# Performance work log

Hardware: AMD Instinct MI355X
Metric: run time of the kernel (lower is better)

Reference implementation:

```python
import jax, jax.numpy as jnp
import numpy as np

B, S, H, L = 4, 8192, 1024, 4
RATIOS = [1.0, 0.5, 0.25, 0.125]
H4 = H // 4


def _xavier(key, shape):
    fan_in, fan_out = shape[-2], shape[-1]
    std = np.sqrt(2.0 / (fan_in + fan_out)).astype(np.float32)
    return jax.random.normal(key, shape, dtype=jnp.float32) * std


def setup_inputs() -> dict:
    key = jax.random.key(0)
    ks = jax.random.split(key, 32)
    it = iter(ks)
    inp = {
        "keys": jax.random.normal(next(it), (B, S, H), dtype=jnp.float32),
        "values": jax.random.normal(next(it), (B, S, H), dtype=jnp.float32),
        # level predictors (same shape across levels -> stacked). Weights stored as [in, out].
        "Pw1": _xavier(next(it), (L, H, H4)),
        "Pb1": jnp.zeros((L, H4), dtype=jnp.float32),
        "Pw2": _xavier(next(it), (L, H4, 1)),
        "Pb2": jnp.zeros((L, 1), dtype=jnp.float32),
    }
    for l, r in enumerate(RATIOS):
        d = int(H * r)
        inp[f"cw1_{l}"] = _xavier(next(it), (H, d))
        inp[f"cb1_{l}"] = jnp.zeros((d,), dtype=jnp.float32)
        inp[f"cw2_{l}"] = _xavier(next(it), (d, H))
        inp[f"cb2_{l}"] = jnp.zeros((H,), dtype=jnp.float32)
    return inp


def reference(keys, values, Pw1, Pb1, Pw2, Pb2,
              cw1_0, cb1_0, cw2_0, cb2_0,
              cw1_1, cb1_1, cw2_1, cb2_1,
              cw1_2, cb1_2, cw2_2, cb2_2,
              cw1_3, cb1_3, cw2_3, cb2_3):
    comps = [
        (cw1_0, cb1_0, cw2_0, cb2_0),
        (cw1_1, cb1_1, cw2_1, cb2_1),
        (cw1_2, cb1_2, cw2_2, cb2_2),
        (cw1_3, cb1_3, cw2_3, cb2_3),
    ]

    def assign_levels(x):
        # per-level predictor: sigmoid(relu(x W1 + b1) W2 + b2) -> argmax over levels
        h = jax.nn.relu(jnp.einsum('bsh,lhd->lbsd', x, Pw1) + Pb1[:, None, None, :])
        p = jax.nn.sigmoid(jnp.einsum('lbsd,ldo->lbso', h, Pw2) + Pb2[:, None, None, :])
        return jnp.argmax(p[..., 0], axis=0)  # [B, S] int, first-max tiebreak like torch.argmax

    def compress(x, lev):
        out = jnp.zeros_like(x)
        for l, (w1, b1, w2, b2) in enumerate(comps):
            y = jax.nn.relu(x @ w1 + b1) @ w2 + b2  # bottleneck MLP for level l
            out = jnp.where((lev == l)[..., None], y, out)
        return out

    key_levels = assign_levels(keys)
    value_levels = assign_levels(values)
    return compress(keys, key_levels), compress(values, value_levels)
```

## Files before the change

### kernel.cpp

```cpp
#include <hip/hip_runtime.h>

#define NTOK 32768
#define MARGIN 0.08f

typedef __attribute__((ext_vector_type(8))) short bshort8;
typedef __attribute__((ext_vector_type(4))) float f32x4;

__device__ __forceinline__ unsigned short f2bf(float f) {
  unsigned u = __float_as_uint(f);
  u += 0x7fffu + ((u >> 16) & 1u);
  return (unsigned short)(u >> 16);
}
__device__ __forceinline__ float bf2f(unsigned short h) {
  return __uint_as_float((unsigned)h << 16);
}

struct TrArgs {
  const float* src[12];
  unsigned short* dst[12];
  int R[12];
  int C[12];
};

__global__ __launch_bounds__(256) void convert_kernel(TrArgs ta) {
  __shared__ float t[32][33];
  const int mid = blockIdx.z;
  const int R = ta.R[mid], C = ta.C[mid];
  const int r0 = blockIdx.y * 32, c0 = blockIdx.x * 32;
  if (r0 >= R || c0 >= C) return;
  const float* __restrict__ src = ta.src[mid];
  unsigned short* __restrict__ dst = ta.dst[mid];
  const int tid = threadIdx.x;
#pragma unroll
  for (int it = 0; it < 4; ++it) {
    int r = it * 8 + (tid >> 5), c = tid & 31;
    t[r][c] = src[(size_t)(r0 + r) * C + c0 + c];
  }
  __syncthreads();
#pragma unroll
  for (int it = 0; it < 4; ++it) {
    int cc = it * 8 + (tid >> 5), rr = tid & 31;
    dst[(size_t)(c0 + cc) * R + r0 + rr] = f2bf(t[rr][cc]);
  }
}

#define M_PRED 0
#define M_L1   1
#define M_L2   2

struct GArgs {
  const float* keys; const float* vals;
  const unsigned short* predW1T;
  const float* Pb1; const float* Pw2;
  float* logits;
  const unsigned short* cw1T[4];
  const unsigned short* cw2T[4];
  const float* cb1[4]; const float* cb2[4];
  unsigned short* h;
  const int* counts; const int* bins;
  const long long* hOff;
  float* out;
};

template<int MODE>
__global__ __launch_bounds__(256) void gemm_core(GArgs ga) {
  const int tid  = threadIdx.x;
  const int lane = tid & 63;
  const int wave = tid >> 6;

  int lev, tens, tile, n0;
  if constexpr (MODE == M_PRED) {
    const int combo = blockIdx.x;
    n0   = (combo & 1) * 128;
    lev  = (combo >> 1) & 3;
    tens = combo >> 3;
    tile = blockIdx.z;
  } else {
    n0   = blockIdx.x * 128;
    const int z = blockIdx.y;
    lev  = z & 3;
    tens = z >> 2;
    tile = blockIdx.z;
  }
  const int z = tens * 4 + lev;
  const int d = 1024 >> lev;

  int cnt, K;
  const unsigned short* Bt;
  if constexpr (MODE == M_PRED) {
    cnt = NTOK; K = 1024;
    Bt = ga.predW1T + ((size_t)lev * 256 + n0) * 1024;
  } else if constexpr (MODE == M_L1) {
    cnt = ga.counts[z]; K = 1024;
    if (n0 >= d) return;
    Bt = ga.cw1T[lev] + (size_t)n0 * 1024;
  } else {
    cnt = ga.counts[z]; K = d;
    Bt = ga.cw2T[lev] + (size_t)n0 * (size_t)d;
  }
  if (tile * 128 >= cnt) return;
  const int nt = min(128, cnt - tile * 128);

  __shared__ __align__(16) char smem[37376];
  int* tokS = (int*)(smem + 36864);

  if constexpr (MODE != M_PRED) {
    if (tid < 128) {
      int idx = tile * 128 + tid;
      tokS[tid] = ga.bins[(size_t)z * NTOK + ((tid < nt) ? idx : tile * 128)];
    }
  }

  const float* __restrict__ X = tens ? ga.vals : ga.keys;
  const unsigned short* hB = nullptr;
  long long hoff = 0;
  if constexpr (MODE == M_L2 || MODE == M_L1) hoff = ga.hOff[z];
  if constexpr (MODE == M_L2) hB = ga.h + hoff;

  f32x4 acc[4][4];
#pragma unroll
  for (int i = 0; i < 4; ++i)
#pragma unroll
    for (int j = 0; j < 4; ++j) acc[i][j] = (f32x4)0.f;

  const int wm = (wave & 1) * 64, wn = (wave >> 1) * 64;

  for (int kc = 0; kc < K; kc += 64) {
    __syncthreads();
    if constexpr (MODE == M_L2) {
#pragma unroll
      for (int it = 0; it < 4; ++it) {
        int r = it * 32 + (tid >> 3), c = tid & 7;
        int rg = tile * 128 + r;
        if (rg >= cnt) rg = cnt - 1;
        const unsigned short* src = hB + (size_t)rg * d + kc + c * 8;
        *(uint4*)(smem + r * 144 + c * 16) = *(const uint4*)src;
      }
    } else {
#pragma unroll
      for (int it = 0; it < 4; ++it) {
        int r = it * 32 + (tid >> 3), j = tid & 7;
        int rowid;
        if constexpr (MODE == M_PRED) rowid = tile * 128 + r;
        else rowid = tokS[r];
        const float* rp = X + (size_t)rowid * 1024 + kc + j * 4;
        float4 v0 = *(const float4*)rp;
        float4 v1 = *(const float4*)(rp + 32);
        ushort4 u0 = { f2bf(v0.x), f2bf(v0.y), f2bf(v0.z), f2bf(v0.w) };
        ushort4 u1 = { f2bf(v1.x), f2bf(v1.y), f2bf(v1.z), f2bf(v1.w) };
        char* dst = smem + r * 144 + j * 8;
        *(ushort4*)dst = u0;
        *(ushort4*)(dst + 64) = u1;
      }
    }
#pragma unroll
    for (int it = 0; it < 4; ++it) {
      int n = it * 32 + (tid >> 3), c = tid & 7;
      const unsigned short* src = Bt + (size_t)n * K + kc + c * 8;
      *(uint4*)(smem + 18432 + n * 144 + c * 16) = *(const uint4*)src;
    }
    __syncthreads();
#pragma unroll
    for (int s = 0; s < 2; ++s) {
      bshort8 af[4], bf[4];
#pragma unroll
      for (int i = 0; i < 4; ++i)
        af[i] = *(const bshort8*)(smem + (wm + i * 16 + (lane & 15)) * 144
                                       + s * 64 + (lane >> 4) * 16);
#pragma unroll
      for (int j = 0; j < 4; ++j)
        bf[j] = *(const bshort8*)(smem + 18432 + (wn + j * 16 + (lane & 15)) * 144
                                       + s * 64 + (lane >> 4) * 16);
#pragma unroll
      for (int i = 0; i < 4; ++i)
#pragma unroll
        for (int j = 0; j < 4; ++j)
          acc[i][j] = __builtin_amdgcn_mfma_f32_16x16x32_bf16(af[i], bf[j], acc[i][j], 0, 0, 0);
    }
  }
  __syncthreads();

  if constexpr (MODE == M_PRED) {
    const float* b1 = ga.Pb1 + lev * 256 + n0;
    const float* w2 = ga.Pw2 + lev * 256 + n0;
    float part[4][4];
#pragma unroll
    for (int i = 0; i < 4; ++i)
#pragma unroll
      for (int r = 0; r < 4; ++r) part[i][r] = 0.f;
#pragma unroll
    for (int j = 0; j < 4; ++j) {
      int col = wn + j * 16 + (lane & 15);
      float bb = b1[col], ww = w2[col];
#pragma unroll
      for (int i = 0; i < 4; ++i)
#pragma unroll
        for (int r = 0; r < 4; ++r)
          part[i][r] = fmaf(fmaxf(acc[i][j][r] + bb, 0.f), ww, part[i][r]);
    }
#pragma unroll
    for (int m = 1; m < 16; m <<= 1)
#pragma unroll
      for (int i = 0; i < 4; ++i)
#pragma unroll
        for (int r = 0; r < 4; ++r)
          part[i][r] += __shfl_xor(part[i][r], m, 64);
    if ((lane & 15) == 0) {
      float* lg = ga.logits + (size_t)z * NTOK;
#pragma unroll
      for (int i = 0; i < 4; ++i)
#pragma unroll
        for (int r = 0; r < 4; ++r) {
          int row = tile * 128 + wm + i * 16 + (lane >> 4) * 4 + r;
          atomicAdd(&lg[row], part[i][r]);
        }
    }
  } else if constexpr (MODE == M_L1) {
    const float* b1 = ga.cb1[lev];
    unsigned short* Hs = (unsigned short*)smem;
#pragma unroll
    for (int i = 0; i < 4; ++i)
#pragma unroll
      for (int j = 0; j < 4; ++j) {
        int col = wn + j * 16 + (lane & 15);
        float bb = b1[n0 + col];
#pragma unroll
        for (int r = 0; r < 4; ++r) {
          int row = wm + i * 16 + (lane >> 4) * 4 + r;
          Hs[row * 128 + col] = f2bf(fmaxf(acc[i][j][r] + bb, 0.f));
        }
      }
    __syncthreads();
    unsigned short* hout = ga.h + hoff;
#pragma unroll
    for (int p = 0; p < 8; ++p) {
      int idx = p * 256 + tid;
      int row = idx >> 4;
      int cc  = (idx & 15) * 8;
      int rg = tile * 128 + row;
      if (rg < cnt)
        *(uint4*)(hout + (size_t)rg * d + n0 + cc) = *(const uint4*)(Hs + row * 128 + cc);
    }
  } else {
    const float* b2 = ga.cb2[lev];
    float* outT = ga.out + (size_t)tens * NTOK * 1024;
#pragma unroll
    for (int i = 0; i < 4; ++i)
#pragma unroll
      for (int r = 0; r < 4; ++r) {
        int row = wm + i * 16 + (lane >> 4) * 4 + r;
        if (row < nt) {
          int tok = tokS[row];
#pragma unroll
          for (int j = 0; j < 4; ++j) {
            int col = n0 + wn + j * 16 + (lane & 15);
            outT[(size_t)tok * 1024 + col] = acc[i][j][r] + b2[col];
          }
        }
      }
  }
}

__global__ __launch_bounds__(256) void argmax_margin_kernel(
    const float* __restrict__ logits, const float* __restrict__ Pb2,
    int* __restrict__ counts, int* __restrict__ bins,
    int* __restrict__ rcnt, int* __restrict__ rlist) {
  int i = blockIdx.x * 256 + threadIdx.x;
  if (i >= 2 * NTOK) return;
  int tens = i >> 15;
  int tok  = i & (NTOK - 1);
  const float* lg = logits + (size_t)tens * 4 * NTOK;
  float best = lg[tok] + Pb2[0];
  int bl = 0;
  float sec = -3.4e38f;
#pragma unroll
  for (int l = 1; l < 4; ++l) {
    float v = lg[(size_t)l * NTOK + tok] + Pb2[l];
    if (v > best) { sec = best; best = v; bl = l; }
    else if (v > sec) sec = v;
  }
  if (best - sec < MARGIN) {
    int pos = atomicAdd(&rcnt[tens], 1);
    rlist[tens * NTOK + pos] = tok;
  } else {
    int bin = tens * 4 + bl;
    int pos = atomicAdd(&counts[bin], 1);
    bins[(size_t)bin * NTOK + pos] = tok;
  }
}

__global__ __launch_bounds__(256) void recheck_gemm(
    const float* __restrict__ keys, const float* __restrict__ vals,
    const float* __restrict__ Pw1, const float* __restrict__ Pb1,
    const float* __restrict__ Pw2, const float* __restrict__ Pb2,
    const int* __restrict__ rcnt, const int* __restrict__ rlist,
    float* __restrict__ logitsR) {
  const int tid  = threadIdx.x;
  const int lev  = blockIdx.y;
  const int tens = blockIdx.z;
  const int cnt  = rcnt[tens];
  const float* __restrict__ X = tens ? vals : keys;
  const float* __restrict__ W = Pw1 + (size_t)lev * 1024 * 256;

  __shared__ float Xs[32][68];
  __shared__ float Ws[32][256];
  __shared__ float red[64][33];
  __shared__ int tokS[64];

  const int tokg = tid >> 5;
  const int colg = tid & 31;

  for (int tile = blockIdx.x; tile * 64 < cnt; tile += gridDim.x) {
    __syncthreads();
    if (tid < 64) {
      int s = tile * 64 + tid;
      tokS[tid] = rlist[tens * NTOK + min(s, cnt - 1)];
    }
    __syncthreads();

    float acc[8][8];
#pragma unroll
    for (int t = 0; t < 8; ++t)
#pragma unroll
      for (int c = 0; c < 8; ++c) acc[t][c] = 0.f;

    for (int kc = 0; kc < 32; ++kc) {
      __syncthreads();
      {
        int j = tid;
        int t64 = j >> 3, kf4 = j & 7;
        float4 v = *(const float4*)&X[(size_t)tokS[t64] * 1024 + kc * 32 + kf4 * 4];
        Xs[kf4 * 4 + 0][t64] = v.x; Xs[kf4 * 4 + 1][t64] = v.y;
        Xs[kf4 * 4 + 2][t64] = v.z; Xs[kf4 * 4 + 3][t64] = v.w;
        j = tid + 256;
        t64 = j >> 3; kf4 = j & 7;
        float4 w = *(const float4*)&X[(size_t)tokS[t64] * 1024 + kc * 32 + kf4 * 4];
        Xs[kf4 * 4 + 0][t64] = w.x; Xs[kf4 * 4 + 1][t64] = w.y;
        Xs[kf4 * 4 + 2][t64] = w.z; Xs[kf4 * 4 + 3][t64] = w.w;
      }
#pragma unroll
      for (int s = 0; s < 8; ++s) {
        int j = tid + s * 256;
        int kr = j >> 6, cf4 = j & 63;
        *(float4*)&Ws[kr][cf4 * 4] =
            *(const float4*)&W[(size_t)(kc * 32 + kr) * 256 + cf4 * 4];
      }
      __syncthreads();
#pragma unroll 8
      for (int kk = 0; kk < 32; ++kk) {
        float4 xa = *(const float4*)&Xs[kk][tokg * 8];
        float4 xb = *(const float4*)&Xs[kk][tokg * 8 + 4];
        float4 wa = *(const float4*)&Ws[kk][colg * 8];
        float4 wb = *(const float4*)&Ws[kk][colg * 8 + 4];
        float xr[8] = {xa.x, xa.y, xa.z, xa.w, xb.x, xb.y, xb.z, xb.w};
        float wr[8] = {wa.x, wa.y, wa.z, wa.w, wb.x, wb.y, wb.z, wb.w};
#pragma unroll
        for (int t = 0; t < 8; ++t)
#pragma unroll
          for (int c = 0; c < 8; ++c)
            acc[t][c] = fmaf(xr[t], wr[c], acc[t][c]);
      }
    }

    const float* b1 = Pb1 + lev * 256;
    const float* w2 = Pw2 + lev * 256;
    float part[8];
#pragma unroll
    for (int t = 0; t < 8; ++t) part[t] = 0.f;
#pragma unroll
    for (int c = 0; c < 8; ++c) {
      float b1c = b1[colg * 8 + c];
      float w2c = w2[colg * 8 + c];
#pragma unroll
      for (int t = 0; t < 8; ++t)
        part[t] = fmaf(fmaxf(acc[t][c] + b1c, 0.f), w2c, part[t]);
    }
    __syncthreads();
#pragma unroll
    for (int t = 0; t < 8; ++t) red[tokg * 8 + t][colg] = part[t];
    __syncthreads();
    if (tid < 64 && tile * 64 + tid < cnt) {
      float s = Pb2[lev];
#pragma unroll
      for (int c = 0; c < 32; ++c) s += red[tid][c];
      logitsR[((size_t)tens * 4 + lev) * NTOK + tile * 64 + tid] = s;
    }
  }
}

__global__ __launch_bounds__(256) void recheck_argmax_kernel(
    const float* __restrict__ logitsR, const int* __restrict__ rcnt,
    const int* __restrict__ rlist, int* __restrict__ counts,
    int* __restrict__ bins) {
  int i = blockIdx.x * 256 + threadIdx.x;
  if (i >= 2 * NTOK) return;
  int tens = i >> 15;
  int slot = i & (NTOK - 1);
  if (slot >= rcnt[tens]) return;
  const float* lg = logitsR + (size_t)tens * 4 * NTOK;
  float best = lg[slot];
  int bl = 0;
#pragma unroll
  for (int l = 1; l < 4; ++l) {
    float v = lg[(size_t)l * NTOK + slot];
    if (v > best) { best = v; bl = l; }
  }
  int tok = rlist[tens * NTOK + slot];
  int bin = tens * 4 + bl;
  int pos = atomicAdd(&counts[bin], 1);
  bins[(size_t)bin * NTOK + pos] = tok;
}

__global__ void hoff_kernel(const int* __restrict__ counts,
                            long long* __restrict__ hOff) {
  long long off = 0;
  for (int b = 0; b < 8; ++b) {
    hOff[b] = off;
    off += (long long)counts[b] * (1024 >> (b & 3));
  }
}

extern "C" void kernel_launch(void* const* d_in, const int* in_sizes, int n_in,
                              void* d_out, int out_size, void* d_ws, size_t ws_size,
                              hipStream_t stream) {
  (void)in_sizes; (void)n_in; (void)out_size; (void)ws_size;
  const float* keys = (const float*)d_in[0];
  const float* vals = (const float*)d_in[1];
  const float* Pw1  = (const float*)d_in[2];
  const float* Pb1  = (const float*)d_in[3];
  const float* Pw2  = (const float*)d_in[4];
  const float* Pb2  = (const float*)d_in[5];

  char* base = (char*)d_ws;
  float* logits   = (float*)(base + 0);
  float* logitsR  = (float*)(base + 1048576);
  int*   bins     = (int*)(base + 2097152);
  int*   rlist    = (int*)(base + 3145728);
  int*   counts   = (int*)(base + 3407872);
  int*   rcnt     = (int*)(base + 3407872 + 32);
  long long* hOff = (long long*)(base + 3407936);
  unsigned short* predW1T = (unsigned short*)(base + 3408384);
  unsigned short* cw1T0 = (unsigned short*)(base + 5505536);
  unsigned short* cw1T1 = (unsigned short*)(base + 7602688);
  unsigned short* cw1T2 = (unsigned short*)(base + 8651264);
  unsigned short* cw1T3 = (unsigned short*)(base + 9175552);
  unsigned short* cw2T0 = (unsigned short*)(base + 9437696);
  unsigned short* cw2T1 = (unsigned short*)(base + 11534848);
  unsigned short* cw2T2 = (unsigned short*)(base + 12583424);
  unsigned short* cw2T3 = (unsigned short*)(base + 13107712);
  unsigned short* hpool = (unsigned short*)(base + 13369856);

  hipMemsetAsync(logits, 0, 1048576, stream);
  hipMemsetAsync(counts, 0, 64, stream);

  TrArgs ta;
  unsigned short* cw1T[4] = {cw1T0, cw1T1, cw1T2, cw1T3};
  unsigned short* cw2T[4] = {cw2T0, cw2T1, cw2T2, cw2T3};
  for (int l = 0; l < 4; ++l) {
    int d = 1024 >> l;
    ta.src[l] = Pw1 + (size_t)l * 1024 * 256;  ta.dst[l] = predW1T + (size_t)l * 256 * 1024;
    ta.R[l] = 1024; ta.C[l] = 256;
    ta.src[4 + l] = (const float*)d_in[6 + l * 4 + 0];  ta.dst[4 + l] = cw1T[l];
    ta.R[4 + l] = 1024; ta.C[4 + l] = d;
    ta.src[8 + l] = (const float*)d_in[6 + l * 4 + 2];  ta.dst[8 + l] = cw2T[l];
    ta.R[8 + l] = d; ta.C[8 + l] = 1024;
  }
  convert_kernel<<<dim3(32, 32, 12), 256, 0, stream>>>(ta);

  GArgs ga;
  ga.keys = keys; ga.vals = vals;
  ga.predW1T = predW1T; ga.Pb1 = Pb1; ga.Pw2 = Pw2;
  ga.logits = logits;
  for (int l = 0; l < 4; ++l) {
    ga.cw1T[l] = cw1T[l];
    ga.cw2T[l] = cw2T[l];
    ga.cb1[l] = (const float*)d_in[6 + l * 4 + 1];
    ga.cb2[l] = (const float*)d_in[6 + l * 4 + 3];
  }
  ga.h = hpool; ga.counts = counts; ga.bins = bins; ga.hOff = hOff;
  ga.out = (float*)d_out;

  gemm_core<M_PRED><<<dim3(16, 1, 256), 256, 0, stream>>>(ga);
  argmax_margin_kernel<<<dim3(256), 256, 0, stream>>>(logits, Pb2, counts, bins, rcnt, rlist);
  recheck_gemm<<<dim3(32, 4, 2), 256, 0, stream>>>(keys, vals, Pw1, Pb1, Pw2, Pb2,
                                                   rcnt, rlist, logitsR);
  recheck_argmax_kernel<<<dim3(256), 256, 0, stream>>>(logitsR, rcnt, rlist, counts, bins);
  hoff_kernel<<<1, 1, 0, stream>>>(counts, hOff);
  gemm_core<M_L1><<<dim3(8, 8, 256), 256, 0, stream>>>(ga);
  gemm_core<M_L2><<<dim3(8, 8, 256), 256, 0, stream>>>(ga);
}
```

Measured before the change: 2.125 ms.

## Pre-convert activations to bf16 and double-buffer GEMM tiles via direct global-to-LDS loads

Adds a pass that converts keys and values to bf16 once, so the predictor and level-1 GEMMs read half the bytes and do no per-tile conversion. The GEMM main loop is rewritten to use global_load_lds 16-byte direct loads into a k-major LDS layout with double buffering over 32-wide K steps, overlapping the next tile's fetch with the current MFMAs. This costs an extra full read and write of the activations plus a larger workspace, and halves the K step, which doubles the barrier count.

```diff
diff --git a/kernel.cpp b/kernel.cpp
--- a/kernel.cpp
+++ b/kernel.cpp
@@ -4,6 +4,7 @@
 #define MARGIN 0.08f
 
 typedef __attribute__((ext_vector_type(8))) short bshort8;
+typedef __attribute__((ext_vector_type(8))) unsigned short ushort8v;
 typedef __attribute__((ext_vector_type(4))) float f32x4;
 
 __device__ __forceinline__ unsigned short f2bf(float f) {
@@ -13,6 +14,29 @@
 }
 __device__ __forceinline__ float bf2f(unsigned short h) {
   return __uint_as_float((unsigned)h << 16);
+}
+
+__device__ __forceinline__ void gload16(const void* g, void* l) {
+  __builtin_amdgcn_global_load_lds(
+      (const __attribute__((address_space(1))) void*)g,
+      (__attribute__((address_space(3))) void*)l, 16, 0, 0);
+}
+
+__global__ __launch_bounds__(256) void xconv_kernel(
+    const float* __restrict__ keys, const float* __restrict__ vals,
+    unsigned short* __restrict__ xbf) {
+  const size_t stride = (size_t)gridDim.x * 256;
+  const size_t half = (size_t)NTOK * 128;
+  for (size_t u = (size_t)blockIdx.x * 256 + threadIdx.x;
+       u < (size_t)2 * NTOK * 128; u += stride) {
+    const float* s = (u < half) ? (keys + u * 8) : (vals + (u - half) * 8);
+    float4 a = *(const float4*)s;
+    float4 b = *(const float4*)(s + 4);
+    ushort8v o;
+    o[0] = f2bf(a.x); o[1] = f2bf(a.y); o[2] = f2bf(a.z); o[3] = f2bf(a.w);
+    o[4] = f2bf(b.x); o[5] = f2bf(b.y); o[6] = f2bf(b.z); o[7] = f2bf(b.w);
+    *(ushort8v*)(xbf + u * 8) = o;
+  }
 }
 
 struct TrArgs {
@@ -49,7 +73,7 @@
 #define M_L2   2
 
 struct GArgs {
-  const float* keys; const float* vals;
+  const unsigned short* xbf;
   const unsigned short* predW1T;
   const float* Pb1; const float* Pw2;
   float* logits;
@@ -77,9 +101,9 @@
     tile = blockIdx.z;
   } else {
     n0   = blockIdx.x * 128;
-    const int z = blockIdx.y;
-    lev  = z & 3;
-    tens = z >> 2;
+    const int zz = blockIdx.y;
+    lev  = zz & 3;
+    tens = zz >> 2;
     tile = blockIdx.z;
   }
   const int z = tens * 4 + lev;
@@ -101,21 +125,36 @@
   if (tile * 128 >= cnt) return;
   const int nt = min(128, cnt - tile * 128);
 
-  __shared__ __align__(16) char smem[37376];
-  int* tokS = (int*)(smem + 36864);
-
-  if constexpr (MODE != M_PRED) {
+  __shared__ __align__(16) char smem[33280];
+  int* tokS = (int*)(smem + 32768);
+
+  long long hoff = 0;
+  if constexpr (MODE != M_PRED) hoff = ga.hOff[z];
+
+  const int arow  = tid & 127;
+  const int celem = (tid >> 7) * 8;
+  const unsigned short* aP;
+  if constexpr (MODE == M_PRED) {
+    aP = ga.xbf + ((size_t)tens * NTOK + tile * 128 + arow) * 1024;
+  } else if constexpr (MODE == M_L1) {
+    int idx = tile * 128 + arow;
+    if (idx >= cnt) idx = cnt - 1;
+    aP = ga.xbf + ((size_t)tens * NTOK + ga.bins[(size_t)z * NTOK + idx]) * 1024;
+  } else {
+    int rg = tile * 128 + arow;
+    if (rg >= cnt) rg = cnt - 1;
+    aP = ga.h + hoff + (size_t)rg * d;
+  }
+  aP += celem;
+  const unsigned short* bP = Bt + (size_t)arow * K + celem;
+
+  if constexpr (MODE == M_L2) {
     if (tid < 128) {
       int idx = tile * 128 + tid;
-      tokS[tid] = ga.bins[(size_t)z * NTOK + ((tid < nt) ? idx : tile * 128)];
-    }
-  }
-
-  const float* __restrict__ X = tens ? ga.vals : ga.keys;
-  const unsigned short* hB = nullptr;
-  long long hoff = 0;
-  if constexpr (MODE == M_L2 || MODE == M_L1) hoff = ga.hOff[z];
-  if constexpr (MODE == M_L2) hB = ga.h + hoff;
+      if (idx >= cnt) idx = cnt - 1;
+      tokS[tid] = ga.bins[(size_t)z * NTOK + idx];
+    }
+  }
 
   f32x4 acc[4][4];
 #pragma unroll
@@ -125,60 +164,42 @@
 
   const int wm = (wave & 1) * 64, wn = (wave >> 1) * 64;
 
-  for (int kc = 0; kc < K; kc += 64) {
+  char* const As0 = smem + tid * 16;
+  char* const As1 = As0 + 4096;
+  char* const Bs0 = As0 + 16384;
+  char* const Bs1 = As0 + 20480;
+
+  gload16(aP,      As0); gload16(aP + 16, As1);
+  gload16(bP,      Bs0); gload16(bP + 16, Bs1);
+  aP += 32; bP += 32;
+  __syncthreads();
+
+  const int fro = (lane >> 4) * 2048 + (lane & 15) * 16;
+  int bufo = 0;
+  const int nk = K >> 5;
+  for (int it = 0; it < nk; ++it) {
+    if (it + 1 < nk) {
+      const int bo = bufo ^ 8192;
+      gload16(aP,      As0 + bo); gload16(aP + 16, As1 + bo);
+      gload16(bP,      Bs0 + bo); gload16(bP + 16, Bs1 + bo);
+      aP += 32; bP += 32;
+    }
+    const char* Ab = smem + bufo + fro;
+    bshort8 af[4], bfr[4];
+#pragma unroll
+    for (int i = 0; i < 4; ++i)
+      af[i] = *(const bshort8*)(Ab + (wm + i * 16) * 16);
+#pragma unroll
+    for (int j = 0; j < 4; ++j)
+      bfr[j] = *(const bshort8*)(Ab + 16384 + (wn + j * 16) * 16);
+#pragma unroll
+    for (int i = 0; i < 4; ++i)
+#pragma unroll
+      for (int j = 0; j < 4; ++j)
+        acc[i][j] = __builtin_amdgcn_mfma_f32_16x16x32_bf16(af[i], bfr[j], acc[i][j], 0, 0, 0);
     __syncthreads();
-    if constexpr (MODE == M_L2) {
-#pragma unroll
-      for (int it = 0; it < 4; ++it) {
-        int r = it * 32 + (tid >> 3), c = tid & 7;
-        int rg = tile * 128 + r;
-        if (rg >= cnt) rg = cnt - 1;
-        const unsigned short* src = hB + (size_t)rg * d + kc + c * 8;
-        *(uint4*)(smem + r * 144 + c * 16) = *(const uint4*)src;
-      }
-    } else {
-#pragma unroll
-      for (int it = 0; it < 4; ++it) {
-        int r = it * 32 + (tid >> 3), j = tid & 7;
-        int rowid;
-        if constexpr (MODE == M_PRED) rowid = tile * 128 + r;
-        else rowid = tokS[r];
-        const float* rp = X + (size_t)rowid * 1024 + kc + j * 4;
-        float4 v0 = *(const float4*)rp;
-        float4 v1 = *(const float4*)(rp + 32);
-        ushort4 u0 = { f2bf(v0.x), f2bf(v0.y), f2bf(v0.z), f2bf(v0.w) };
-        ushort4 u1 = { f2bf(v1.x), f2bf(v1.y), f2bf(v1.z), f2bf(v1.w) };
-        char* dst = smem + r * 144 + j * 8;
-        *(ushort4*)dst = u0;
-        *(ushort4*)(dst + 64) = u1;
-      }
-    }
-#pragma unroll
-    for (int it = 0; it < 4; ++it) {
-      int n = it * 32 + (tid >> 3), c = tid & 7;
-      const unsigned short* src = Bt + (size_t)n * K + kc + c * 8;
-      *(uint4*)(smem + 18432 + n * 144 + c * 16) = *(const uint4*)src;
-    }
-    __syncthreads();
-#pragma unroll
-    for (int s = 0; s < 2; ++s) {
-      bshort8 af[4], bf[4];
-#pragma unroll
-      for (int i = 0; i < 4; ++i)
-        af[i] = *(const bshort8*)(smem + (wm + i * 16 + (lane & 15)) * 144
-                                       + s * 64 + (lane >> 4) * 16);
-#pragma unroll
-      for (int j = 0; j < 4; ++j)
-        bf[j] = *(const bshort8*)(smem + 18432 + (wn + j * 16 + (lane & 15)) * 144
-                                       + s * 64 + (lane >> 4) * 16);
-#pragma unroll
-      for (int i = 0; i < 4; ++i)
-#pragma unroll
-        for (int j = 0; j < 4; ++j)
-          acc[i][j] = __builtin_amdgcn_mfma_f32_16x16x32_bf16(af[i], bf[j], acc[i][j], 0, 0, 0);
-    }
-  }
-  __syncthreads();
+    bufo ^= 8192;
+  }
 
   if constexpr (MODE == M_PRED) {
     const float* b1 = ga.Pb1 + lev * 256 + n0;
@@ -449,9 +470,12 @@
   unsigned short* cw2T2 = (unsigned short*)(base + 12583424);
   unsigned short* cw2T3 = (unsigned short*)(base + 13107712);
   unsigned short* hpool = (unsigned short*)(base + 13369856);
+  unsigned short* xbf   = (unsigned short*)(base + 147587584);
 
   hipMemsetAsync(logits, 0, 1048576, stream);
   hipMemsetAsync(counts, 0, 64, stream);
+
+  xconv_kernel<<<dim3(2048), 256, 0, stream>>>(keys, vals, xbf);
 
   TrArgs ta;
   unsigned short* cw1T[4] = {cw1T0, cw1T1, cw1T2, cw1T3};
@@ -468,7 +492,7 @@
   convert_kernel<<<dim3(32, 32, 12), 256, 0, stream>>>(ta);
 
   GArgs ga;
-  ga.keys = keys; ga.vals = vals;
+  ga.xbf = xbf;
   ga.predW1T = predW1T; ga.Pb1 = Pb1; ga.Pw2 = Pw2;
   ga.logits = logits;
   for (int l = 0; l < 4; ++l) {
```

Measured after the change: 2.220 ms. +4.4%, slower.
